# Optimization experiments

Measured on AMD Instinct MI355X. Metric: run time of the kernel, lower is better.

## Reference

```python
import jax, jax.numpy as jnp
import numpy as np

D_MODEL, N_HEADS, D_HEAD = 1024, 16, 64
INIT_RANGE = 0.02
IGNORE = -100000.0


def setup_inputs() -> dict:
    key = jax.random.key(0)
    ks = jax.random.split(key, 5)
    x = jax.random.normal(ks[0], (2, 2048, D_MODEL), dtype=jnp.float32)
    W_Q = jax.random.normal(ks[1], (N_HEADS, D_MODEL, D_HEAD), dtype=jnp.float32) * INIT_RANGE
    W_K = jax.random.normal(ks[2], (N_HEADS, D_MODEL, D_HEAD), dtype=jnp.float32) * INIT_RANGE
    W_V = jax.random.normal(ks[3], (N_HEADS, D_MODEL, D_HEAD), dtype=jnp.float32) * INIT_RANGE
    W_O = jax.random.normal(ks[4], (N_HEADS, D_HEAD, D_MODEL), dtype=jnp.float32) * INIT_RANGE
    b_Q = jnp.zeros((N_HEADS, D_HEAD), dtype=jnp.float32)
    b_K = jnp.zeros((N_HEADS, D_HEAD), dtype=jnp.float32)
    b_V = jnp.zeros((N_HEADS, D_HEAD), dtype=jnp.float32)
    b_O = jnp.zeros((D_MODEL,), dtype=jnp.float32)
    return {"normalized_resid_pre": x, "W_Q": W_Q, "b_Q": b_Q, "W_K": W_K,
            "b_K": b_K, "W_V": W_V, "b_V": b_V, "W_O": W_O, "b_O": b_O}


def reference(normalized_resid_pre, W_Q, b_Q, W_K, b_K, W_V, b_V, W_O, b_O):
    x = normalized_resid_pre  # [b, s, d_model]
    q = jnp.einsum('bsd,hde->bshe', x, W_Q) + b_Q  # [b, s, h, d_head]
    k = jnp.einsum('bsd,hde->bshe', x, W_K) + b_K
    v = jnp.einsum('bsd,hde->bshe', x, W_V) + b_V
    scores = jnp.einsum('bqhe,bkhe->bhqk', q, k) / jnp.sqrt(jnp.float32(D_HEAD))
    S = scores.shape[-1]
    causal = jnp.triu(jnp.ones((S, S), dtype=bool), k=1)  # True above diagonal
    scores = jnp.where(causal, jnp.float32(IGNORE), scores)
    pattern = jax.nn.softmax(scores, axis=-1)
    z = jnp.einsum('bhqk,bkhe->bqhe', pattern, v)
    out = jnp.einsum('bqhe,hed->bqd', z, W_O) + b_O
    return out
```

## Files before the change

### kernel.cpp

```cpp
#include <hip/hip_runtime.h>
#include <math.h>

#define DMODEL 1024
#define NHEADS 16
#define DHEAD 64
#define SEQL 2048
#define NBATCH 2
#define MROWS (NBATCH*SEQL)
#define NQKV (3*DMODEL)

typedef __attribute__((ext_vector_type(8))) short bf8;
typedef __attribute__((ext_vector_type(4))) float f4;

__device__ __forceinline__ unsigned short f2b(float f) {
  union { float f; unsigned int u; } v; v.f = f;
  unsigned int r = v.u + 0x7FFFu + ((v.u >> 16) & 1u);
  return (unsigned short)(r >> 16);
}

__device__ __forceinline__ f4 mfma16(bf8 a, bf8 b, f4 c) {
  return __builtin_amdgcn_mfma_f32_16x16x32_bf16(a, b, c, 0, 0, 0);
}

__device__ __forceinline__ void gload16(const void* g, void* l) {
  __builtin_amdgcn_global_load_lds(
      (const __attribute__((address_space(1))) unsigned int*)g,
      (__attribute__((address_space(3))) unsigned int*)l, 16, 0, 0);
}


__global__ __launch_bounds__(256) void k_f32_to_bf16(const float* __restrict__ in,
                                                     unsigned short* __restrict__ out, int n4) {
  int i = blockIdx.x * 256 + threadIdx.x;
  if (i < n4) {
    float4 v = ((const float4*)in)[i];
    ushort4 o;
    o.x = f2b(v.x); o.y = f2b(v.y); o.z = f2b(v.z); o.w = f2b(v.w);
    ((ushort4*)out)[i] = o;
  }
}

__global__ __launch_bounds__(256) void k_pack_wqkv(
    const float* __restrict__ Wq, const float* __restrict__ Wk, const float* __restrict__ Wv,
    const float* __restrict__ bq, const float* __restrict__ bk, const float* __restrict__ bv,
    unsigned short* __restrict__ Wt, float* __restrict__ biasq) {
  __shared__ float tile[64][65];
  int tid = threadIdx.x;
  int dt = blockIdx.x, h = blockIdx.y, p = blockIdx.z;
  const float* W = (p == 0) ? Wq : ((p == 1) ? Wk : Wv);
  #pragma unroll
  for (int j = 0; j < 16; j++) {
    int idx = tid + j * 256;
    int dd = idx >> 6, e = idx & 63;
    tile[dd][e] = W[(size_t)(h * DMODEL + dt * 64 + dd) * DHEAD + e];
  }
  __syncthreads();
  #pragma unroll
  for (int j = 0; j < 16; j++) {
    int idx = tid + j * 256;
    int e = idx >> 6, dd = idx & 63;
    Wt[(size_t)(p * DMODEL + h * 64 + e) * DMODEL + dt * 64 + dd] = f2b(tile[dd][e]);
  }
  if (dt == 0 && tid < 64) {
    const float* bsel = (p == 0) ? bq : ((p == 1) ? bk : bv);
    biasq[p * DMODEL + h * 64 + tid] = bsel[h * 64 + tid];
  }
}

__global__ __launch_bounds__(256) void k_pack_wo(const float* __restrict__ Wo,
                                                 unsigned short* __restrict__ Wot) {
  __shared__ float tile[64][65];
  int tid = threadIdx.x;
  int het = blockIdx.x, dmt = blockIdx.y;
  #pragma unroll
  for (int j = 0; j < 16; j++) {
    int idx = tid + j * 256;
    int r = idx >> 6, c = idx & 63;
    tile[r][c] = Wo[(size_t)(het * 64 + r) * DMODEL + dmt * 64 + c];
  }
  __syncthreads();
  #pragma unroll
  for (int j = 0; j < 16; j++) {
    int idx = tid + j * 256;
    int rr = idx >> 6, cc = idx & 63;
    Wot[(size_t)(dmt * 64 + rr) * DMODEL + het * 64 + cc] = f2b(tile[cc][rr]);
  }
}


template<int N, int K, bool OUTF32>
__global__ __launch_bounds__(256) void k_gemm_bt(
    const unsigned short* __restrict__ A, const unsigned short* __restrict__ Bt,
    const float* __restrict__ bias, void* __restrict__ Cp) {
  __shared__ unsigned short As[128 * 64];
  __shared__ unsigned short Bs[128 * 64];
  int tid = threadIdx.x;
  int lane = tid & 63, w = tid >> 6;
  int wr = w >> 1, wc = w & 1;
  int lr = lane & 15, lg = lane >> 4;
  int m0 = blockIdx.x * 128, n0 = blockIdx.y * 128;
  int srow = w * 8 + (lane >> 3);
  int scol = ((lane & 7) ^ (lane >> 3)) * 8;
  f4 acc[4][4] = {};
  for (int k0 = 0; k0 < K; k0 += 64) {
    #pragma unroll
    for (int it = 0; it < 4; it++) {
      int row = it * 32 + srow;
      gload16(&A[(size_t)(m0 + row) * K + k0 + scol], &As[(it * 256 + w * 64) * 8]);
      gload16(&Bt[(size_t)(n0 + row) * K + k0 + scol], &Bs[(it * 256 + w * 64) * 8]);
    }
    __syncthreads();
    #pragma unroll
    for (int kk = 0; kk < 2; kk++) {
      bf8 af[4], bfv[4];
      #pragma unroll
      for (int i = 0; i < 4; i++) {
        int ra = wr * 64 + i * 16 + lr;
        int rb = wc * 64 + i * 16 + lr;
        af[i]  = *(const bf8*)(&As[ra * 64 + (((kk * 4 + lg) ^ (ra & 7)) * 8)]);
        bfv[i] = *(const bf8*)(&Bs[rb * 64 + (((kk * 4 + lg) ^ (rb & 7)) * 8)]);
      }
      #pragma unroll
      for (int i = 0; i < 4; i++)
        #pragma unroll
        for (int j = 0; j < 4; j++)
          acc[i][j] = mfma16(af[i], bfv[j], acc[i][j]);
    }
    __syncthreads();
  }
  #pragma unroll
  for (int i = 0; i < 4; i++)
    #pragma unroll
    for (int j = 0; j < 4; j++) {
      int col = n0 + wc * 64 + j * 16 + lr;
      float bv = bias[col];
      #pragma unroll
      for (int r = 0; r < 4; r++) {
        int row = m0 + wr * 64 + i * 16 + lg * 4 + r;
        float v = acc[i][j][r] + bv;
        if (OUTF32) ((float*)Cp)[(size_t)row * N + col] = v;
        else ((unsigned short*)Cp)[(size_t)row * N + col] = f2b(v);
      }
    }
}


#define KP 72
#define SWZ(r, c) ((r) * KP + ((c) ^ ((((r) >> 3) & 7) << 3)))

__global__ __launch_bounds__(256) void k_attn(const unsigned short* __restrict__ qkv,
                                              unsigned short* __restrict__ zb) {
  __shared__ unsigned short Ks[64 * KP];
  __shared__ unsigned short Vt[64 * KP];
  __shared__ unsigned short Pl[4][32 * KP];
  int tid = threadIdx.x;
  int lane = tid & 63, w = tid >> 6;
  int lr = lane & 15, lg = lane >> 4;
  int tlo = blockIdx.x;
  int thi = 31 - tlo;
  int bh = blockIdx.y;
  int b = bh >> 4, h = bh & 15;
  int qb[2] = { tlo * 64 + w * 16, thi * 64 + w * 16 };
  const size_t rowbase = (size_t)b * SEQL;

  bf8 qf_[2][2];
  #pragma unroll
  for (int i = 0; i < 2; i++)
    #pragma unroll
    for (int kd = 0; kd < 2; kd++)
      qf_[i][kd] = *(const bf8*)(&qkv[(rowbase + qb[i] + lr) * NQKV + h * DHEAD + kd * 32 + lg * 8]);

  f4 accz[2][4] = {};
  float m_[2][4], l_[2][4];
  #pragma unroll
  for (int i = 0; i < 2; i++)
    #pragma unroll
    for (int r = 0; r < 4; r++) { m_[i][r] = -1e30f; l_[i][r] = 0.f; }

  int nkv = thi + 1;
  for (int tt = 0; tt < nkv; tt++) {
    int kv0 = tt << 6;
    #pragma unroll
    for (int cc = 0; cc < 2; cc++) {
      int c = tid + cc * 256;
      int kv = c >> 3, dc = (c & 7) * 8;
      *(int4*)(&Ks[SWZ(kv, dc)]) =
          *(const int4*)(&qkv[(rowbase + kv0 + kv) * NQKV + DMODEL + h * DHEAD + dc]);
      int4 vvi = *(const int4*)(&qkv[(rowbase + kv0 + kv) * NQKV + 2 * DMODEL + h * DHEAD + dc]);
      const unsigned short* vv = (const unsigned short*)&vvi;
      #pragma unroll
      for (int i2 = 0; i2 < 8; i2++) Vt[SWZ(dc + i2, kv)] = vv[i2];
    }
    __syncthreads();
    bool act0 = (tt <= tlo);
    f4 s[2][4] = {};
    #pragma unroll
    for (int kd = 0; kd < 2; kd++) {
      bf8 kf_[4];
      #pragma unroll
      for (int j = 0; j < 4; j++)
        kf_[j] = *(const bf8*)(&Ks[SWZ(j * 16 + lr, kd * 32 + lg * 8)]);
      #pragma unroll
      for (int i = 0; i < 2; i++) {
        if (i == 0 && !act0) continue;
        #pragma unroll
        for (int j = 0; j < 4; j++)
          s[i][j] = mfma16(qf_[i][kd], kf_[j], s[i][j]);
      }
    }
    #pragma unroll
    for (int i = 0; i < 2; i++) {
      if (i == 0 && !act0) continue;
      #pragma unroll
      for (int j = 0; j < 4; j++)
        #pragma unroll
        for (int r = 0; r < 4; r++) {
          int row = qb[i] + lg * 4 + r;
          int col = kv0 + j * 16 + lr;
          float sv = s[i][j][r] * 0.125f;
          s[i][j][r] = (col > row) ? -1e30f : sv;
        }
      #pragma unroll
      for (int r = 0; r < 4; r++) {
        float mx = fmaxf(fmaxf(s[i][0][r], s[i][1][r]), fmaxf(s[i][2][r], s[i][3][r]));
        #pragma unroll
        for (int d = 1; d < 16; d <<= 1) mx = fmaxf(mx, __shfl_xor(mx, d));
        float mn = fmaxf(m_[i][r], mx);
        float al = __expf(m_[i][r] - mn);
        m_[i][r] = mn;
        l_[i][r] *= al;
        #pragma unroll
        for (int e = 0; e < 4; e++) accz[i][e][r] *= al;
        float rs = 0.f;
        #pragma unroll
        for (int j = 0; j < 4; j++) {
          float pv = __expf(s[i][j][r] - mn);
          s[i][j][r] = pv;
          rs += pv;
        }
        #pragma unroll
        for (int d = 1; d < 16; d <<= 1) rs += __shfl_xor(rs, d);
        l_[i][r] += rs;
      }
      #pragma unroll
      for (int j = 0; j < 4; j++)
        #pragma unroll
        for (int r = 0; r < 4; r++)
          Pl[w][SWZ(i * 16 + lg * 4 + r, j * 16 + lr)] = f2b(s[i][j][r]);
    }
    #pragma unroll
    for (int ks = 0; ks < 2; ks++) {
      bf8 vb[4];
      #pragma unroll
      for (int e = 0; e < 4; e++)
        vb[e] = *(const bf8*)(&Vt[SWZ(e * 16 + lr, ks * 32 + lg * 8)]);
      #pragma unroll
      for (int i = 0; i < 2; i++) {
        if (i == 0 && !act0) continue;
        bf8 pa = *(const bf8*)(&Pl[w][SWZ(i * 16 + lr, ks * 32 + lg * 8)]);
        #pragma unroll
        for (int e = 0; e < 4; e++)
          accz[i][e] = mfma16(pa, vb[e], accz[i][e]);
      }
    }
    __syncthreads();
  }
  #pragma unroll
  for (int i = 0; i < 2; i++)
    #pragma unroll
    for (int r = 0; r < 4; r++) {
      float inv = 1.0f / l_[i][r];
      size_t row = rowbase + qb[i] + lg * 4 + r;
      #pragma unroll
      for (int e = 0; e < 4; e++)
        zb[row * DMODEL + h * DHEAD + e * 16 + lr] = f2b(accz[i][e][r] * inv);
    }
}


extern "C" void kernel_launch(void* const* d_in, const int* in_sizes, int n_in,
                              void* d_out, int out_size, void* d_ws, size_t ws_size,
                              hipStream_t stream) {
  const float* x  = (const float*)d_in[0];
  const float* Wq = (const float*)d_in[1];
  const float* bq = (const float*)d_in[2];
  const float* Wk = (const float*)d_in[3];
  const float* bk = (const float*)d_in[4];
  const float* Wv = (const float*)d_in[5];
  const float* bv = (const float*)d_in[6];
  const float* Wo = (const float*)d_in[7];
  const float* bo = (const float*)d_in[8];

  char* ws = (char*)d_ws;
  unsigned short* xb    = (unsigned short*)(ws);
  unsigned short* wqkvt = (unsigned short*)(ws + 8388608);
  float*          biasq = (float*)(ws + 8388608 + 6291456);
  unsigned short* qkv   = (unsigned short*)(ws + 8388608 + 6291456 + 16384);
  unsigned short* wot   = (unsigned short*)(ws + 8388608 + 6291456 + 16384 + 25165824);
  unsigned short* zbuf  = xb;

  k_f32_to_bf16<<<(MROWS * DMODEL / 4 + 255) / 256, 256, 0, stream>>>(x, xb, MROWS * DMODEL / 4);
  k_pack_wqkv<<<dim3(16, 16, 3), 256, 0, stream>>>(Wq, Wk, Wv, bq, bk, bv, wqkvt, biasq);
  k_pack_wo<<<dim3(16, 16), 256, 0, stream>>>(Wo, wot);
  k_gemm_bt<NQKV, DMODEL, false><<<dim3(32, 24), 256, 0, stream>>>(xb, wqkvt, biasq, qkv);
  k_attn<<<dim3(16, 32), 256, 0, stream>>>(qkv, zbuf);
  k_gemm_bt<DMODEL, DMODEL, true><<<dim3(32, 8), 256, 0, stream>>>(zbuf, wot, bo, (float*)d_out);
}
```

Before: 247.4 us.

## Restructure attention kernel around 32x32 MFMA with register-resident P and lazy rescale

Rewrites the attention kernel to use 32x32x16 bf16 MFMA on 128-query-row tiles, one 32-row slice per wave. It computes S transposed (K as the A operand), so P can be packed with v_cvt_pk_bf16 and lane-swapped into the PV operand in registers instead of round-tripping through LDS. K tiles are loaded with global_load_lds into an XOR-swizzled buffer. Online-softmax rescaling is skipped unless the running max grows by more than a threshold. This adds cross-lane shuffles, an LDS broadcast of the rescale factors, and a launch_bounds occupancy hint, and drops the earlier paired low/high tile balancing.

```diff
diff --git a/kernel.cpp b/kernel.cpp
--- a/kernel.cpp
+++ b/kernel.cpp
@@ -11,6 +11,7 @@
 
 typedef __attribute__((ext_vector_type(8))) short bf8;
 typedef __attribute__((ext_vector_type(4))) float f4;
+typedef __attribute__((ext_vector_type(16))) float f16v;
 
 __device__ __forceinline__ unsigned short f2b(float f) {
   union { float f; unsigned int u; } v; v.f = f;
@@ -20,6 +21,16 @@
 
 __device__ __forceinline__ f4 mfma16(bf8 a, bf8 b, f4 c) {
   return __builtin_amdgcn_mfma_f32_16x16x32_bf16(a, b, c, 0, 0, 0);
+}
+
+__device__ __forceinline__ f16v mfma32(bf8 a, bf8 b, f16v c) {
+  return __builtin_amdgcn_mfma_f32_32x32x16_bf16(a, b, c, 0, 0, 0);
+}
+
+__device__ __forceinline__ unsigned cvtpk(float lo, float hi) {
+  unsigned r;
+  asm("v_cvt_pk_bf16_f32 %0, %1, %2" : "=v"(r) : "v"(lo), "v"(hi));
+  return r;
 }
 
 __device__ __forceinline__ void gload16(const void* g, void* l) {
@@ -145,136 +156,134 @@
 }
 
 
-#define KP 72
-#define SWZ(r, c) ((r) * KP + ((c) ^ ((((r) >> 3) & 7) << 3)))
-
-__global__ __launch_bounds__(256) void k_attn(const unsigned short* __restrict__ qkv,
-                                              unsigned short* __restrict__ zb) {
-  __shared__ unsigned short Ks[64 * KP];
-  __shared__ unsigned short Vt[64 * KP];
-  __shared__ unsigned short Pl[4][32 * KP];
+#define VKP 72
+#define VSWZ(r, c) ((r) * VKP + ((c) ^ ((((r) >> 3) & 7) << 3)))
+
+__global__ __launch_bounds__(256, 2) void k_attn(const unsigned short* __restrict__ qkv,
+                                                 unsigned short* __restrict__ zb) {
+  __shared__ __align__(16) unsigned short Ks[64 * 64];
+  __shared__ __align__(16) unsigned short Vt[64 * VKP];
+  __shared__ float Lb[4][32];
   int tid = threadIdx.x;
   int lane = tid & 63, w = tid >> 6;
-  int lr = lane & 15, lg = lane >> 4;
-  int tlo = blockIdx.x;
-  int thi = 31 - tlo;
+  int l31 = lane & 31, h5 = lane >> 5;
+  int qt = 15 - blockIdx.x;
   int bh = blockIdx.y;
   int b = bh >> 4, h = bh & 15;
-  int qb[2] = { tlo * 64 + w * 16, thi * 64 + w * 16 };
+  int qw = qt * 128 + w * 32;
   const size_t rowbase = (size_t)b * SEQL;
-
-  bf8 qf_[2][2];
-  #pragma unroll
-  for (int i = 0; i < 2; i++)
-    #pragma unroll
-    for (int kd = 0; kd < 2; kd++)
-      qf_[i][kd] = *(const bf8*)(&qkv[(rowbase + qb[i] + lr) * NQKV + h * DHEAD + kd * 32 + lg * 8]);
-
-  f4 accz[2][4] = {};
-  float m_[2][4], l_[2][4];
-  #pragma unroll
-  for (int i = 0; i < 2; i++)
-    #pragma unroll
-    for (int r = 0; r < 4; r++) { m_[i][r] = -1e30f; l_[i][r] = 0.f; }
-
-  int nkv = thi + 1;
+  int qg = qw + l31;
+
+  bf8 qf[4];
+  #pragma unroll
+  for (int ds = 0; ds < 4; ds++)
+    qf[ds] = *(const bf8*)(&qkv[(rowbase + qg) * NQKV + h * DHEAD + ds * 16 + h5 * 8]);
+
+  f16v zacc0 = {}, zacc1 = {};
+  float m = -1e30f, lsum = 0.f;
+
+  int sr = tid >> 3;
+  int scc = ((tid & 7) ^ (sr & 7)) * 8;
+
+  int nkv = 2 * qt + 2;
   for (int tt = 0; tt < nkv; tt++) {
-    int kv0 = tt << 6;
+    int kv0 = tt * 64;
+    #pragma unroll
+    for (int it = 0; it < 2; it++)
+      gload16(&qkv[(rowbase + kv0 + it * 32 + sr) * NQKV + DMODEL + h * DHEAD + scc],
+              &Ks[(it * 256 + w * 64) * 8]);
     #pragma unroll
     for (int cc = 0; cc < 2; cc++) {
       int c = tid + cc * 256;
       int kv = c >> 3, dc = (c & 7) * 8;
-      *(int4*)(&Ks[SWZ(kv, dc)]) =
-          *(const int4*)(&qkv[(rowbase + kv0 + kv) * NQKV + DMODEL + h * DHEAD + dc]);
       int4 vvi = *(const int4*)(&qkv[(rowbase + kv0 + kv) * NQKV + 2 * DMODEL + h * DHEAD + dc]);
       const unsigned short* vv = (const unsigned short*)&vvi;
       #pragma unroll
-      for (int i2 = 0; i2 < 8; i2++) Vt[SWZ(dc + i2, kv)] = vv[i2];
+      for (int i2 = 0; i2 < 8; i2++) Vt[VSWZ(dc + i2, kv)] = vv[i2];
     }
     __syncthreads();
-    bool act0 = (tt <= tlo);
-    f4 s[2][4] = {};
-    #pragma unroll
-    for (int kd = 0; kd < 2; kd++) {
-      bf8 kf_[4];
-      #pragma unroll
-      for (int j = 0; j < 4; j++)
-        kf_[j] = *(const bf8*)(&Ks[SWZ(j * 16 + lr, kd * 32 + lg * 8)]);
-      #pragma unroll
-      for (int i = 0; i < 2; i++) {
-        if (i == 0 && !act0) continue;
-        #pragma unroll
-        for (int j = 0; j < 4; j++)
-          s[i][j] = mfma16(qf_[i][kd], kf_[j], s[i][j]);
+    #pragma unroll
+    for (int t32 = 0; t32 < 2; t32++) {
+      int kb = kv0 + t32 * 32;
+      if (kb <= qw + 31) {
+        f16v sa = {};
+        int ar = t32 * 32 + l31;
+        #pragma unroll
+        for (int ds = 0; ds < 4; ds++) {
+          bf8 kf = *(const bf8*)(&Ks[ar * 64 + (((ds * 2 + h5) ^ (ar & 7)) * 8)]);
+          sa = mfma32(kf, qf[ds], sa);
+        }
+        float p[16];
+        int diffh = qg - kb - 4 * h5;
+        if (kb + 31 > qw) {
+          #pragma unroll
+          for (int r = 0; r < 16; r++) {
+            int kc4 = (r & 3) + 8 * (r >> 2);
+            p[r] = (kc4 > diffh) ? -1e30f : sa[r] * 0.125f;
+          }
+        } else {
+          #pragma unroll
+          for (int r = 0; r < 16; r++) p[r] = sa[r] * 0.125f;
+        }
+        float pmax = p[0];
+        #pragma unroll
+        for (int r = 1; r < 16; r++) pmax = fmaxf(pmax, p[r]);
+        pmax = fmaxf(pmax, __shfl_xor(pmax, 32));
+        if (!__all(pmax - m <= 8.0f)) {
+          float mn = fmaxf(m, pmax);
+          float al = __expf(m - mn);
+          Lb[w][l31] = al;
+          m = mn;
+          lsum *= al;
+          #pragma unroll
+          for (int r = 0; r < 16; r++) {
+            float alr = Lb[w][(r & 3) + 8 * (r >> 2) + 4 * h5];
+            zacc0[r] *= alr;
+            zacc1[r] *= alr;
+          }
+        }
+        float ps = 0.f;
+        #pragma unroll
+        for (int r = 0; r < 16; r++) { p[r] = __expf(p[r] - m); ps += p[r]; }
+        ps += __shfl_xor(ps, 32);
+        lsum += ps;
+        unsigned X1 = cvtpk(p[0], p[1]),   Y1 = cvtpk(p[4], p[5]);
+        unsigned X2 = cvtpk(p[2], p[3]),   Y2 = cvtpk(p[6], p[7]);
+        unsigned X3 = cvtpk(p[8], p[9]),   Y3 = cvtpk(p[12], p[13]);
+        unsigned X4 = cvtpk(p[10], p[11]), Y4 = cvtpk(p[14], p[15]);
+        unsigned Xs1 = __shfl_xor((int)X1, 32), Ys1 = __shfl_xor((int)Y1, 32);
+        unsigned Xs2 = __shfl_xor((int)X2, 32), Ys2 = __shfl_xor((int)Y2, 32);
+        unsigned Xs3 = __shfl_xor((int)X3, 32), Ys3 = __shfl_xor((int)Y3, 32);
+        unsigned Xs4 = __shfl_xor((int)X4, 32), Ys4 = __shfl_xor((int)Y4, 32);
+        union { bf8 v; unsigned u[4]; } pa0, pa1;
+        pa0.u[0] = h5 ? Ys1 : X1;  pa0.u[2] = h5 ? Y1 : Xs1;
+        pa0.u[1] = h5 ? Ys2 : X2;  pa0.u[3] = h5 ? Y2 : Xs2;
+        pa1.u[0] = h5 ? Ys3 : X3;  pa1.u[2] = h5 ? Y3 : Xs3;
+        pa1.u[1] = h5 ? Ys4 : X4;  pa1.u[3] = h5 ? Y4 : Xs4;
+        #pragma unroll
+        for (int e = 0; e < 2; e++) {
+          int vr = e * 32 + l31;
+          int fv = ((vr >> 3) & 7) << 3;
+          f16v& zr = e ? zacc1 : zacc0;
+          #pragma unroll
+          for (int ks = 0; ks < 2; ks++) {
+            bf8 vb = *(const bf8*)(&Vt[vr * VKP + ((t32 * 32 + ks * 16 + h5 * 8) ^ fv)]);
+            zr = mfma32(ks ? pa1.v : pa0.v, vb, zr);
+          }
+        }
       }
     }
-    #pragma unroll
-    for (int i = 0; i < 2; i++) {
-      if (i == 0 && !act0) continue;
-      #pragma unroll
-      for (int j = 0; j < 4; j++)
-        #pragma unroll
-        for (int r = 0; r < 4; r++) {
-          int row = qb[i] + lg * 4 + r;
-          int col = kv0 + j * 16 + lr;
-          float sv = s[i][j][r] * 0.125f;
-          s[i][j][r] = (col > row) ? -1e30f : sv;
-        }
-      #pragma unroll
-      for (int r = 0; r < 4; r++) {
-        float mx = fmaxf(fmaxf(s[i][0][r], s[i][1][r]), fmaxf(s[i][2][r], s[i][3][r]));
-        #pragma unroll
-        for (int d = 1; d < 16; d <<= 1) mx = fmaxf(mx, __shfl_xor(mx, d));
-        float mn = fmaxf(m_[i][r], mx);
-        float al = __expf(m_[i][r] - mn);
-        m_[i][r] = mn;
-        l_[i][r] *= al;
-        #pragma unroll
-        for (int e = 0; e < 4; e++) accz[i][e][r] *= al;
-        float rs = 0.f;
-        #pragma unroll
-        for (int j = 0; j < 4; j++) {
-          float pv = __expf(s[i][j][r] - mn);
-          s[i][j][r] = pv;
-          rs += pv;
-        }
-        #pragma unroll
-        for (int d = 1; d < 16; d <<= 1) rs += __shfl_xor(rs, d);
-        l_[i][r] += rs;
-      }
-      #pragma unroll
-      for (int j = 0; j < 4; j++)
-        #pragma unroll
-        for (int r = 0; r < 4; r++)
-          Pl[w][SWZ(i * 16 + lg * 4 + r, j * 16 + lr)] = f2b(s[i][j][r]);
-    }
-    #pragma unroll
-    for (int ks = 0; ks < 2; ks++) {
-      bf8 vb[4];
-      #pragma unroll
-      for (int e = 0; e < 4; e++)
-        vb[e] = *(const bf8*)(&Vt[SWZ(e * 16 + lr, ks * 32 + lg * 8)]);
-      #pragma unroll
-      for (int i = 0; i < 2; i++) {
-        if (i == 0 && !act0) continue;
-        bf8 pa = *(const bf8*)(&Pl[w][SWZ(i * 16 + lr, ks * 32 + lg * 8)]);
-        #pragma unroll
-        for (int e = 0; e < 4; e++)
-          accz[i][e] = mfma16(pa, vb[e], accz[i][e]);
-      }
-    }
     __syncthreads();
   }
-  #pragma unroll
-  for (int i = 0; i < 2; i++)
-    #pragma unroll
-    for (int r = 0; r < 4; r++) {
-      float inv = 1.0f / l_[i][r];
-      size_t row = rowbase + qb[i] + lg * 4 + r;
-      #pragma unroll
-      for (int e = 0; e < 4; e++)
-        zb[row * DMODEL + h * DHEAD + e * 16 + lr] = f2b(accz[i][e][r] * inv);
-    }
+  Lb[w][l31] = 1.0f / lsum;
+  #pragma unroll
+  for (int r = 0; r < 16; r++) {
+    int crow = (r & 3) + 8 * (r >> 2) + 4 * h5;
+    float inv = Lb[w][crow];
+    size_t row = rowbase + qw + crow;
+    zb[row * DMODEL + h * DHEAD + l31] = f2b(zacc0[r] * inv);
+    zb[row * DMODEL + h * DHEAD + 32 + l31] = f2b(zacc1[r] * inv);
+  }
 }
 
 
```

Result: faster. 232.2 us (-6.2%).
